# Kernel tuning notes

Hardware: AMD Instinct MI355X
Metric: run time of the kernel (lower is better)

## Reference

```python
import jax, jax.numpy as jnp
import numpy as np
import math

B, L, D, NH, FF, NL = 4, 512, 512, 8, 2048, 4
DS, DC, DI, DTR = 64, 4, 1024, 32  # mamba: d_state, d_conv, d_inner=2*D, dt_rank=ceil(D/16)
HD = D // NH


def _layer_norm(x, g, b):
    m = x.mean(-1, keepdims=True)
    v = ((x - m) ** 2).mean(-1, keepdims=True)
    return (x - m) / jnp.sqrt(v + 1e-5) * g + b


def _pos_encode(x):
    Lx, Dx = x.shape[1], x.shape[2]
    pos = jnp.arange(Lx, dtype=jnp.float32)[:, None]
    div = jnp.exp(jnp.arange(0, Dx, 2, dtype=jnp.float32) * (-math.log(10000.0) / Dx))
    ang = pos * div  # (L, D/2)
    pe = jnp.stack([jnp.sin(ang), jnp.cos(ang)], -1).reshape(Lx, Dx)  # interleaved sin/cos
    return x + pe[None]


def _mha(x, w_qkv, b_qkv, w_o, b_o):
    Bx, Lx, Dx = x.shape
    qkv = x @ w_qkv.T + b_qkv
    q, k, v = jnp.split(qkv, 3, -1)
    heads = lambda t: t.reshape(Bx, Lx, NH, HD).transpose(0, 2, 1, 3)
    q, k, v = heads(q), heads(k), heads(v)
    s = jnp.einsum('bhqd,bhkd->bhqk', q, k) / math.sqrt(HD)
    p = jax.nn.softmax(s, -1)
    o = jnp.einsum('bhqk,bhkd->bhqd', p, v).transpose(0, 2, 1, 3).reshape(Bx, Lx, Dx)
    return o @ w_o.T + b_o


def _mamba(x, in_w, conv_w, conv_b, xproj_w, dt_w, dt_b, A_log, D_skip, out_w):
    Bx, Lx, _ = x.shape
    xz = x @ in_w.T  # (B, L, 2*DI)
    xc, z = jnp.split(xz, 2, -1)
    # depthwise causal conv1d
    xc = jax.lax.conv_general_dilated(xc.transpose(0, 2, 1), conv_w[:, None, :], (1,), [(DC - 1, 0)], feature_group_count=DI, dimension_numbers=('NCH', 'OIH', 'NCH'))
    xc = jax.nn.silu((xc + conv_b[None, :, None]).transpose(0, 2, 1))  # (B, L, DI)
    x_dbl = xc @ xproj_w.T
    dt, Bm, Cm = jnp.split(x_dbl, [DTR, DTR + DS], -1)
    dt = jax.nn.softplus(dt @ dt_w.T + dt_b)  # (B, L, DI)
    A = -jnp.exp(A_log)  # (DI, DS)

    def step(h, t):
        dt_t, B_t, C_t, u_t = t  # (B,DI),(B,DS),(B,DS),(B,DI)
        h = jnp.exp(dt_t[:, :, None] * A) * h + (dt_t * u_t)[:, :, None] * B_t[:, None, :]
        return h, jnp.einsum('bdn,bn->bd', h, C_t)

    h0 = jnp.zeros((Bx, DI, DS), x.dtype)
    xs = (dt.transpose(1, 0, 2), Bm.transpose(1, 0, 2), Cm.transpose(1, 0, 2), xc.transpose(1, 0, 2))
    _, ys = jax.lax.scan(step, h0, xs)
    y = ys.transpose(1, 0, 2) + xc * D_skip
    y = y * jax.nn.silu(z)
    return y @ out_w.T


def setup_inputs():
    key = jax.random.key(0)
    ks = iter(jax.random.split(key, 32))
    def rn(shape, s=0.02):
        return jax.random.normal(next(ks), shape, jnp.float32) * s
    return dict(
        src=jax.random.normal(next(ks), (B, L, D), jnp.float32),
        attn_w_qkv=rn((NL, 3 * D, D)), attn_b_qkv=jnp.zeros((NL, 3 * D)),
        attn_w_o=rn((NL, D, D)), attn_b_o=jnp.zeros((NL, D)),
        ffn_w1=rn((NL, FF, D)), ffn_b1=jnp.zeros((NL, FF)),
        ffn_w2=rn((NL, D, FF)), ffn_b2=jnp.zeros((NL, D)),
        norm1_g=jnp.ones((NL, D)), norm1_b=jnp.zeros((NL, D)),
        in_proj_w=rn((NL, 2 * DI, D)), conv_w=rn((NL, DI, DC), 0.2), conv_b=jnp.zeros((NL, DI)),
        x_proj_w=rn((NL, DTR + 2 * DS, DI)), dt_proj_w=rn((NL, DI, DTR), 0.1), dt_proj_b=jnp.full((NL, DI), -4.0),
        A_log=jnp.broadcast_to(jnp.log(jnp.arange(1, DS + 1, dtype=jnp.float32)), (NL, DI, DS)) + 0.0,
        D_skip=jnp.ones((NL, DI)), out_proj_w=rn((NL, D, DI)),
        normf_g=jnp.ones((D,)), normf_b=jnp.zeros((D,)))


def reference(src, attn_w_qkv, attn_b_qkv, attn_w_o, attn_b_o, ffn_w1, ffn_b1, ffn_w2, ffn_b2, norm1_g, norm1_b, in_proj_w, conv_w, conv_b, x_proj_w, dt_proj_w, dt_proj_b, A_log, D_skip, out_proj_w, normf_g, normf_b):
    x = _pos_encode(src)
    for i in range(NL):
        a = _mha(x, attn_w_qkv[i], attn_b_qkv[i], attn_w_o[i], attn_b_o[i])
        m = _mamba(x, in_proj_w[i], conv_w[i], conv_b[i], x_proj_w[i], dt_proj_w[i], dt_proj_b[i], A_log[i], D_skip[i], out_proj_w[i])
        h = a + m
        h = jax.nn.relu(h @ ffn_w1[i].T + ffn_b1[i]) @ ffn_w2[i].T + ffn_b2[i]
        x = _layer_norm(h, norm1_g[i], norm1_b[i])  # norm1(dropout(ffn(attn+mamba))), dropout=identity
    return _layer_norm(x, normf_g, normf_b)
```

## Files before the change

### kernel.cpp

```cpp
#include <hip/hip_runtime.h>
#include <cmath>


typedef __attribute__((ext_vector_type(8))) __bf16 bf16x8;
typedef __attribute__((ext_vector_type(4))) __bf16 bf16x4;
typedef __attribute__((ext_vector_type(4))) float f32x4;

#define DEV static __device__ __forceinline__

DEV float wave_sum(float x) {
#pragma unroll
  for (int o = 32; o; o >>= 1) x += __shfl_xor(x, o, 64);
  return x;
}
DEV float wave_max(float x) {
#pragma unroll
  for (int o = 32; o; o >>= 1) x = fmaxf(x, __shfl_xor(x, o, 64));
  return x;
}

__global__ void cvt_kernel(const float* __restrict__ s, __bf16* __restrict__ d, int n4) {
  int i = blockIdx.x * 256 + threadIdx.x;
  if (i < n4) {
    float4 v = ((const float4*)s)[i];
    bf16x4 r = {(__bf16)v.x, (__bf16)v.y, (__bf16)v.z, (__bf16)v.w};
    *(bf16x4*)(d + (size_t)i * 4) = r;
  }
}

__global__ void pe_kernel(const float* __restrict__ src, __bf16* __restrict__ xb) {
  int idx = blockIdx.x * 256 + threadIdx.x;
  int d = idx & 511;
  int l = (idx >> 9) & 511;
  float ang = (float)l * expf((float)(d & ~1) * (-9.210340371976184f / 512.f));
  float pe = (d & 1) ? cosf(ang) : sinf(ang);
  xb[idx] = (__bf16)(src[idx] + pe);
}

struct GemmArgs {
  const __bf16* A; const __bf16* W;
  const float* bias; const float* add;
  float* Cf; __bf16* Cb;
  long long sAzb, sAzh, sWzb, sWzh, sADzb, sADzh, sCfzb, sCfzh, sCbzb, sCbzh;
  int lda, ldw, ldad, ldcf, ldcb;
  int M, N, K, ZH;
  float alpha; int act;
  int ct;
};

__global__ __launch_bounds__(64) void gemm_kernel(GemmArgs g) {
  const int lane = threadIdx.x;
  const int m0 = blockIdx.x * 64, n0 = blockIdx.y * 64;
  const int zb = blockIdx.z / g.ZH, zh = blockIdx.z % g.ZH;
  const __bf16* A = g.A + zb * g.sAzb + zh * g.sAzh;
  const __bf16* W = g.W + zb * g.sWzb + zh * g.sWzh;
  const int fr = lane & 15;
  const int fk = (lane >> 4) * 8;
  const __bf16* pa[4]; const __bf16* pw[4];
#pragma unroll
  for (int i = 0; i < 4; ++i) {
    int ra = m0 + i * 16 + fr;
    pa[i] = A + (size_t)ra * g.lda + fk;
    int rw = n0 + i * 16 + fr; if (rw > g.N - 1) rw = g.N - 1;
    pw[i] = W + (size_t)rw * g.ldw + fk;
  }
  f32x4 acc[4][4] = {};
  for (int k0 = 0; k0 < g.K; k0 += 32) {
    bf16x8 af[4], wf[4];
#pragma unroll
    for (int i = 0; i < 4; ++i) af[i] = *(const bf16x8*)(pa[i] + k0);
#pragma unroll
    for (int j = 0; j < 4; ++j) wf[j] = *(const bf16x8*)(pw[j] + k0);
#pragma unroll
    for (int i = 0; i < 4; ++i)
#pragma unroll
      for (int j = 0; j < 4; ++j)
        acc[i][j] = __builtin_amdgcn_mfma_f32_16x16x32_bf16(af[i], wf[j], acc[i][j], 0, 0, 0);
  }
  const float* addp = g.add ? g.add + zb * g.sADzb + zh * g.sADzh : nullptr;
  float* cf = g.Cf ? g.Cf + zb * g.sCfzb + zh * g.sCfzh : nullptr;
  __bf16* cb = g.Cb ? g.Cb + zb * g.sCbzb + zh * g.sCbzh : nullptr;
  const int rbase = m0 + (lane >> 4) * 4;
#pragma unroll
  for (int i = 0; i < 4; ++i) {
#pragma unroll
    for (int j = 0; j < 4; ++j) {
      int col = n0 + j * 16 + fr;
      if (col < g.N) {
#pragma unroll
        for (int r = 0; r < 4; ++r) {
          int row = rbase + i * 16 + r;
          float v = acc[i][j][r] * g.alpha;
          if (g.bias) v += g.bias[col];
          if (addp) v += addp[(size_t)row * g.ldad + col];
          if (g.act == 1) v = fmaxf(v, 0.f);
          else if (g.act == 2) v = (v > 20.f) ? v : log1pf(expf(v));
          if (cf) {
            if (g.ct) cf[(size_t)col * g.ldcf + row] = v;
            else      cf[(size_t)row * g.ldcf + col] = v;
          }
          if (cb) cb[(size_t)row * g.ldcb + col] = (__bf16)v;
        }
      }
    }
  }
}

static void launch_gemm(hipStream_t st,
    const __bf16* A, int lda, long long sAzb, long long sAzh,
    const __bf16* W, int ldw, long long sWzb, long long sWzh,
    const float* bias,
    const float* add, int ldad, long long sADzb, long long sADzh,
    float* Cf, int ldcf, long long sCfzb, long long sCfzh,
    __bf16* Cb, int ldcb, long long sCbzb, long long sCbzh,
    int M, int N, int K, int Z, int ZH, float alpha, int act, int ct = 0) {
  GemmArgs g;
  g.A = A; g.W = W; g.bias = bias; g.add = add; g.Cf = Cf; g.Cb = Cb;
  g.sAzb = sAzb; g.sAzh = sAzh; g.sWzb = sWzb; g.sWzh = sWzh;
  g.sADzb = sADzb; g.sADzh = sADzh; g.sCfzb = sCfzb; g.sCfzh = sCfzh;
  g.sCbzb = sCbzb; g.sCbzh = sCbzh;
  g.lda = lda; g.ldw = ldw; g.ldad = ldad; g.ldcf = ldcf; g.ldcb = ldcb;
  g.M = M; g.N = N; g.K = K; g.ZH = ZH; g.alpha = alpha; g.act = act; g.ct = ct;
  dim3 grid(M / 64, (N + 63) / 64, Z);
  gemm_kernel<<<grid, 64, 0, st>>>(g);
}

__global__ __launch_bounds__(256) void gemm_sk_kernel(GemmArgs g) {
  __shared__ float red[2][64 * 66];
  const int tid = threadIdx.x;
  const int lane = tid & 63;
  const int wid = tid >> 6;
  const int m0 = blockIdx.x * 64, n0 = blockIdx.y * 64;
  const int zb = blockIdx.z / g.ZH, zh = blockIdx.z % g.ZH;
  const __bf16* A = g.A + zb * g.sAzb + zh * g.sAzh;
  const __bf16* W = g.W + zb * g.sWzb + zh * g.sWzh;
  const int fr = lane & 15;
  const int fk = (lane >> 4) * 8;
  const int kbase = wid * (g.K >> 2);
  const __bf16* pa[4]; const __bf16* pw[4];
#pragma unroll
  for (int i = 0; i < 4; ++i) {
    int ra = m0 + i * 16 + fr;
    pa[i] = A + (size_t)ra * g.lda + kbase + fk;
    int rw = n0 + i * 16 + fr; if (rw > g.N - 1) rw = g.N - 1;
    pw[i] = W + (size_t)rw * g.ldw + kbase + fk;
  }
  f32x4 acc[4][4] = {};
  const int kend = g.K >> 2;
  for (int k0 = 0; k0 < kend; k0 += 32) {
    bf16x8 af[4], wf[4];
#pragma unroll
    for (int i = 0; i < 4; ++i) af[i] = *(const bf16x8*)(pa[i] + k0);
#pragma unroll
    for (int j = 0; j < 4; ++j) wf[j] = *(const bf16x8*)(pw[j] + k0);
#pragma unroll
    for (int i = 0; i < 4; ++i)
#pragma unroll
      for (int j = 0; j < 4; ++j)
        acc[i][j] = __builtin_amdgcn_mfma_f32_16x16x32_bf16(af[i], wf[j], acc[i][j], 0, 0, 0);
  }
  float* buf0 = &red[0][0];
  float* buf1 = &red[1][0];
  auto store_acc = [&](float* buf) {
#pragma unroll
    for (int i = 0; i < 4; ++i)
#pragma unroll
      for (int j = 0; j < 4; ++j) {
        int rl = i * 16 + ((lane >> 4) << 2);
        int cl = j * 16 + fr;
#pragma unroll
        for (int r = 0; r < 4; ++r) buf[(rl + r) * 66 + cl] = acc[i][j][r];
      }
  };
  auto add_acc = [&](const float* buf) {
#pragma unroll
    for (int i = 0; i < 4; ++i)
#pragma unroll
      for (int j = 0; j < 4; ++j) {
        int rl = i * 16 + ((lane >> 4) << 2);
        int cl = j * 16 + fr;
#pragma unroll
        for (int r = 0; r < 4; ++r) acc[i][j][r] += buf[(rl + r) * 66 + cl];
      }
  };
  if (wid == 1) store_acc(buf0);
  if (wid == 3) store_acc(buf1);
  __syncthreads();
  if (wid == 0) add_acc(buf0);
  if (wid == 2) add_acc(buf1);
  __syncthreads();
  if (wid == 2) store_acc(buf0);
  __syncthreads();
  if (wid == 0) { add_acc(buf0); store_acc(buf0); }
  __syncthreads();
  const int rl = tid >> 2;
  const int c0l = (tid & 3) * 16;
  const int row = m0 + rl;
  const float* addp = g.add ? g.add + zb * g.sADzb + zh * g.sADzh : nullptr;
  float* cf = g.Cf ? g.Cf + zb * g.sCfzb + zh * g.sCfzh : nullptr;
  __bf16* cb = g.Cb ? g.Cb + zb * g.sCbzb + zh * g.sCbzh : nullptr;
  float v[16];
#pragma unroll
  for (int k = 0; k < 16; ++k) {
    float x = buf0[rl * 66 + c0l + k] * g.alpha;
    int col = n0 + c0l + k;
    if (col < g.N) {
      if (g.bias) x += g.bias[col];
      if (addp) x += addp[(size_t)row * g.ldad + col];
      if (g.act == 1) x = fmaxf(x, 0.f);
      else if (g.act == 2) x = (x > 20.f) ? x : log1pf(expf(x));
    }
    v[k] = x;
  }
  if (n0 + c0l + 15 < g.N) {
    if (cf) {
      float* p = cf + (size_t)row * g.ldcf + n0 + c0l;
#pragma unroll
      for (int k = 0; k < 4; ++k) *(float4*)(p + k * 4) = *(float4*)(v + k * 4);
    }
    if (cb) {
      __bf16* p = cb + (size_t)row * g.ldcb + n0 + c0l;
#pragma unroll
      for (int h = 0; h < 2; ++h) {
        bf16x8 r;
#pragma unroll
        for (int k = 0; k < 8; ++k) r[k] = (__bf16)v[h * 8 + k];
        *(bf16x8*)(p + h * 8) = r;
      }
    }
  } else {
#pragma unroll
    for (int k = 0; k < 16; ++k) {
      int col = n0 + c0l + k;
      if (col < g.N) {
        if (cf) cf[(size_t)row * g.ldcf + col] = v[k];
        if (cb) cb[(size_t)row * g.ldcb + col] = (__bf16)v[k];
      }
    }
  }
}

static void launch_gemm_sk(hipStream_t st,
    const __bf16* A, int lda, long long sAzb, long long sAzh,
    const __bf16* W, int ldw, long long sWzb, long long sWzh,
    const float* bias,
    const float* add, int ldad, long long sADzb, long long sADzh,
    float* Cf, int ldcf, long long sCfzb, long long sCfzh,
    __bf16* Cb, int ldcb, long long sCbzb, long long sCbzh,
    int M, int N, int K, int Z, int ZH, float alpha, int act) {
  GemmArgs g;
  g.A = A; g.W = W; g.bias = bias; g.add = add; g.Cf = Cf; g.Cb = Cb;
  g.sAzb = sAzb; g.sAzh = sAzh; g.sWzb = sWzb; g.sWzh = sWzh;
  g.sADzb = sADzb; g.sADzh = sADzh; g.sCfzb = sCfzb; g.sCfzh = sCfzh;
  g.sCbzb = sCbzb; g.sCbzh = sCbzh;
  g.lda = lda; g.ldw = ldw; g.ldad = ldad; g.ldcf = ldcf; g.ldcb = ldcb;
  g.M = M; g.N = N; g.K = K; g.ZH = ZH; g.alpha = alpha; g.act = act; g.ct = 0;
  dim3 grid(M / 64, (N + 63) / 64, Z);
  gemm_sk_kernel<<<grid, 256, 0, st>>>(g);
}

__global__ __launch_bounds__(256) void transpose_v_kernel(const __bf16* __restrict__ qkv,
                                                          __bf16* __restrict__ vt) {
  int bh = blockIdx.x, b = bh >> 3, h = bh & 7;
  const __bf16* s = qkv + (size_t)b * 512 * 1536 + 1024 + h * 64;
  __bf16* dst = vt + (size_t)bh * 64 * 512;
  __shared__ __align__(16) __bf16 tile[64 * 72];
  int tid = threadIdx.x;
  for (int l0 = 0; l0 < 512; l0 += 64) {
    __syncthreads();
#pragma unroll
    for (int it = 0; it < 2; ++it) {
      int idx = tid + it * 256;
      int l = idx >> 3, dc = (idx & 7) * 8;
      *(uint4*)&tile[l * 72 + dc] = *(const uint4*)(s + (size_t)(l0 + l) * 1536 + dc);
    }
    __syncthreads();
#pragma unroll
    for (int it = 0; it < 2; ++it) {
      int idx = tid + it * 256;
      int dd = idx >> 3, lc = (idx & 7) * 8;
      __align__(16) __bf16 tmp[8];
#pragma unroll
      for (int j = 0; j < 8; ++j) tmp[j] = tile[(lc + j) * 72 + dd];
      *(uint4*)(dst + (size_t)dd * 512 + l0 + lc) = *(uint4*)tmp;
    }
  }
}

__global__ __launch_bounds__(256) void softmax_kernel(const float* __restrict__ S,
                                                      __bf16* __restrict__ P) {
  int row = blockIdx.x * 4 + (threadIdx.x >> 6);
  int lane = threadIdx.x & 63;
  const float* sp = S + (size_t)row * 512 + lane * 8;
  float v[8];
  *(float4*)(v) = *(const float4*)(sp);
  *(float4*)(v + 4) = *(const float4*)(sp + 4);
  float m = v[0];
#pragma unroll
  for (int k = 1; k < 8; ++k) m = fmaxf(m, v[k]);
  m = wave_max(m);
  float s = 0.f;
#pragma unroll
  for (int k = 0; k < 8; ++k) { v[k] = __expf(v[k] - m); s += v[k]; }
  s = wave_sum(s);
  float inv = 1.f / s;
  bf16x8 r;
#pragma unroll
  for (int k = 0; k < 8; ++k) r[k] = (__bf16)(v[k] * inv);
  *(bf16x8*)(P + (size_t)row * 512 + lane * 8) = r;
}

__global__ __launch_bounds__(256) void conv_silu_t_kernel(
    const float* __restrict__ xz, const float* __restrict__ cw, const float* __restrict__ cb,
    __bf16* __restrict__ xcb, float* __restrict__ uT, float* __restrict__ s1T) {
  int c0 = blockIdx.x * 64, t0 = blockIdx.y * 64, b = blockIdx.z;
  __shared__ float su[64][65];
  __shared__ float sz[64][65];
  int c = threadIdx.x & 63;
  int tr = threadIdx.x >> 6;
  int ch = c0 + c;
  float w0 = cw[ch * 4 + 0], w1 = cw[ch * 4 + 1], w2 = cw[ch * 4 + 2], w3 = cw[ch * 4 + 3];
  float bias = cb[ch];
#pragma unroll 4
  for (int it = 0; it < 16; ++it) {
    int tt = it * 4 + tr;
    int t = t0 + tt;
    const float* col = xz + (size_t)b * 512 * 2048 + ch;
    float acc = bias;
    if (t >= 3) {
      acc = fmaf(w0, col[(size_t)(t - 3) * 2048], acc);
      acc = fmaf(w1, col[(size_t)(t - 2) * 2048], acc);
      acc = fmaf(w2, col[(size_t)(t - 1) * 2048], acc);
    } else {
      if (t - 3 >= 0) acc = fmaf(w0, col[(size_t)(t - 3) * 2048], acc);
      if (t - 2 >= 0) acc = fmaf(w1, col[(size_t)(t - 2) * 2048], acc);
      if (t - 1 >= 0) acc = fmaf(w2, col[(size_t)(t - 1) * 2048], acc);
    }
    acc = fmaf(w3, col[(size_t)t * 2048], acc);
    float u = acc / (1.f + __expf(-acc));
    su[tt][c] = u;
    xcb[(size_t)(b * 512 + t) * 1024 + ch] = (__bf16)u;
    float zv = col[(size_t)t * 2048 + 1024];
    sz[tt][c] = zv / (1.f + __expf(-zv));
  }
  __syncthreads();
  int c2 = threadIdx.x >> 2;
  int tb = (threadIdx.x & 3) * 16;
  size_t g = (size_t)(c0 + c2) * 2048 + (size_t)b * 512 + t0 + tb;
#pragma unroll
  for (int i = 0; i < 16; ++i) {
    uT[g + i] = su[tb + i][c2];
    s1T[g + i] = sz[tb + i][c2];
  }
}

__global__ __launch_bounds__(256) void scan_p1_kernel(
    const float* __restrict__ dtT, const float* __restrict__ uT,
    const float* __restrict__ xdbl, const float* __restrict__ A_log,
    float* __restrict__ Aprod, float* __restrict__ hend) {
  int w = (blockIdx.x * 256 + threadIdx.x) >> 6;
  int lane = threadIdx.x & 63;
  int c = w & 7, di = (w >> 3) & 1023, b = w >> 13;
  float aL2 = -__expf(A_log[di * 64 + lane]) * 1.4426950408889634f;
  int t0 = c * 64;
  size_t sbase = (size_t)di * 2048 + (size_t)b * 512 + t0;
  const float* dtp = dtT + sbase;
  const float* up = uT + sbase;
  const float* bp = xdbl + ((size_t)(b * 512 + t0)) * 160 + 32 + lane;
  float h = 0.f, sdt = 0.f;
#pragma unroll 8
  for (int s = 0; s < 64; ++s) {
    float dtv = dtp[s];
    float duv = dtv * up[s];
    float Bv = bp[(size_t)s * 160];
    float dec = exp2f(dtv * aL2);
    sdt += dtv;
    h = fmaf(dec, h, duv * Bv);
  }
  size_t o = (size_t)w * 64 + lane;
  Aprod[o] = exp2f(sdt * aL2);
  hend[o] = h;
}

__global__ __launch_bounds__(256) void scan_p2_kernel(
    const float* __restrict__ Aprod, const float* __restrict__ hend,
    float* __restrict__ hstart) {
  int w = (blockIdx.x * 256 + threadIdx.x) >> 6;
  int lane = threadIdx.x & 63;
  float h = 0.f;
  size_t base = (size_t)w * 8 * 64 + lane;
#pragma unroll
  for (int c = 0; c < 8; ++c) {
    size_t o = base + (size_t)c * 64;
    hstart[o] = h;
    h = fmaf(Aprod[o], h, hend[o]);
  }
}

__global__ __launch_bounds__(128) void scan_p3_kernel(
    const float* __restrict__ dtT, const float* __restrict__ uT,
    const float* __restrict__ s1T, const float* __restrict__ xdbl,
    const float* __restrict__ A_log, const float* __restrict__ Dskip,
    const float* __restrict__ hstart, __bf16* __restrict__ yT) {
  __shared__ float Q[2][32][65];
  int wl = threadIdx.x >> 6;
  int w = (blockIdx.x * 128 + threadIdx.x) >> 6;
  int lane = threadIdx.x & 63;
  int c = w & 7, di = (w >> 3) & 1023, b = w >> 13;
  float aL2 = -__expf(A_log[di * 64 + lane]) * 1.4426950408889634f;
  int t0 = c * 64;
  size_t sbase = (size_t)di * 2048 + (size_t)b * 512 + t0;
  const float* dtp = dtT + sbase;
  const float* up = uT + sbase;
  const float* bp = xdbl + ((size_t)(b * 512 + t0)) * 160 + 32 + lane;
  const float* cp = bp + 64;
  float h = hstart[(size_t)w * 64 + lane];
  float y = 0.f;
#pragma unroll 8
  for (int s = 0; s < 32; ++s) {
    float dtv = dtp[s];
    float duv = dtv * up[s];
    float Bv = bp[(size_t)s * 160];
    float Cv = cp[(size_t)s * 160];
    float dec = exp2f(dtv * aL2);
    h = fmaf(dec, h, duv * Bv);
    Q[wl][s][lane] = h * Cv;
  }
  if (lane < 32) {
    const float* row = &Q[wl][lane][0];
    float a0 = 0.f, a1 = 0.f, a2 = 0.f, a3 = 0.f;
#pragma unroll
    for (int k = 0; k < 64; k += 4) {
      a0 += row[k]; a1 += row[k + 1]; a2 += row[k + 2]; a3 += row[k + 3];
    }
    y = (a0 + a1) + (a2 + a3);
  }
#pragma unroll 8
  for (int s = 32; s < 64; ++s) {
    float dtv = dtp[s];
    float duv = dtv * up[s];
    float Bv = bp[(size_t)s * 160];
    float Cv = cp[(size_t)s * 160];
    float dec = exp2f(dtv * aL2);
    h = fmaf(dec, h, duv * Bv);
    Q[wl][s - 32][lane] = h * Cv;
  }
  if (lane >= 32) {
    const float* row = &Q[wl][lane - 32][0];
    float a0 = 0.f, a1 = 0.f, a2 = 0.f, a3 = 0.f;
#pragma unroll
    for (int k = 0; k < 64; k += 4) {
      a0 += row[k]; a1 += row[k + 1]; a2 += row[k + 2]; a3 += row[k + 3];
    }
    y = (a0 + a1) + (a2 + a3);
  }
  float ue = up[lane];
  float s1e = s1T[sbase + lane];
  yT[sbase + lane] = (__bf16)((y + ue * Dskip[di]) * s1e);
}

__global__ __launch_bounds__(256) void transpose_y_kernel(const __bf16* __restrict__ src,
                                                          __bf16* __restrict__ dst) {
  int r0 = blockIdx.x * 64;
  int c0 = blockIdx.y * 64;
  __shared__ __align__(16) __bf16 tile[64 * 72];
  int tid = threadIdx.x;
#pragma unroll
  for (int it = 0; it < 2; ++it) {
    int idx = tid + it * 256;
    int r = idx >> 3, cc = (idx & 7) * 8;
    *(uint4*)&tile[r * 72 + cc] = *(const uint4*)(src + (size_t)(r0 + r) * 2048 + c0 + cc);
  }
  __syncthreads();
#pragma unroll
  for (int it = 0; it < 2; ++it) {
    int idx = tid + it * 256;
    int cr = idx >> 3, rc = (idx & 7) * 8;
    __align__(16) __bf16 tmp[8];
#pragma unroll
    for (int j = 0; j < 8; ++j) tmp[j] = tile[(rc + j) * 72 + cr];
    *(uint4*)(dst + (size_t)(c0 + cr) * 1024 + r0 + rc) = *(uint4*)tmp;
  }
}

__global__ __launch_bounds__(256) void layernorm_kernel(const float* __restrict__ in,
    const float* __restrict__ g, const float* __restrict__ b,
    float* __restrict__ outf, __bf16* __restrict__ outb) {
  int row = blockIdx.x * 4 + (threadIdx.x >> 6);
  int lane = threadIdx.x & 63;
  const float* p = in + (size_t)row * 512 + lane * 8;
  float v[8];
  *(float4*)(v) = *(const float4*)(p);
  *(float4*)(v + 4) = *(const float4*)(p + 4);
  float s = 0.f;
#pragma unroll
  for (int k = 0; k < 8; ++k) s += v[k];
  float mean = wave_sum(s) * (1.f / 512.f);
  float q = 0.f;
#pragma unroll
  for (int k = 0; k < 8; ++k) { float d = v[k] - mean; q += d * d; }
  float var = wave_sum(q) * (1.f / 512.f);
  float rs = rsqrtf(var + 1e-5f);
  float gv[8], bv[8];
  *(float4*)(gv) = *(const float4*)(g + lane * 8);
  *(float4*)(gv + 4) = *(const float4*)(g + lane * 8 + 4);
  *(float4*)(bv) = *(const float4*)(b + lane * 8);
  *(float4*)(bv + 4) = *(const float4*)(b + lane * 8 + 4);
  float o[8];
#pragma unroll
  for (int k = 0; k < 8; ++k) o[k] = (v[k] - mean) * rs * gv[k] + bv[k];
  if (outf) {
    float* op = outf + (size_t)row * 512 + lane * 8;
    *(float4*)(op) = *(const float4*)(o);
    *(float4*)(op + 4) = *(const float4*)(o + 4);
  }
  if (outb) {
    bf16x8 r;
#pragma unroll
    for (int k = 0; k < 8; ++k) r[k] = (__bf16)o[k];
    *(bf16x8*)(outb + (size_t)row * 512 + lane * 8) = r;
  }
}

extern "C" void kernel_launch(void* const* d_in, const int* in_sizes, int n_in,
                              void* d_out, int out_size, void* d_ws, size_t ws_size,
                              hipStream_t stream) {
  const float* src    = (const float*)d_in[0];
  const float* w_qkv  = (const float*)d_in[1];
  const float* b_qkv  = (const float*)d_in[2];
  const float* w_o    = (const float*)d_in[3];
  const float* b_o    = (const float*)d_in[4];
  const float* w1     = (const float*)d_in[5];
  const float* b1     = (const float*)d_in[6];
  const float* w2     = (const float*)d_in[7];
  const float* b2     = (const float*)d_in[8];
  const float* n1g    = (const float*)d_in[9];
  const float* n1b    = (const float*)d_in[10];
  const float* w_in   = (const float*)d_in[11];
  const float* conv_w = (const float*)d_in[12];
  const float* conv_b = (const float*)d_in[13];
  const float* w_xp   = (const float*)d_in[14];
  const float* w_dt   = (const float*)d_in[15];
  const float* b_dt   = (const float*)d_in[16];
  const float* A_log  = (const float*)d_in[17];
  const float* D_skip = (const float*)d_in[18];
  const float* w_out  = (const float*)d_in[19];
  const float* nfg    = (const float*)d_in[20];
  const float* nfb    = (const float*)d_in[21];
  (void)in_sizes; (void)n_in; (void)out_size; (void)ws_size;

  char* ws = (char*)d_ws;
  __bf16* Wqkv = (__bf16*)(ws + 0);
  __bf16* Wo   = (__bf16*)(ws + 6291456);
  __bf16* W1   = (__bf16*)(ws + 8388608);
  __bf16* W2   = (__bf16*)(ws + 16777216);
  __bf16* Win  = (__bf16*)(ws + 25165824);
  __bf16* Wxp  = (__bf16*)(ws + 33554432);
  __bf16* Wdt  = (__bf16*)(ws + 34865152);
  __bf16* Wout = (__bf16*)(ws + 35127296);
  __bf16* xb16 = (__bf16*)(ws + 39321600);
  float*  xf32 = (float*)(ws + 41418752);
  __bf16* qkvb = (__bf16*)(ws + 45613056);
  __bf16* vt   = (__bf16*)(ws + 51904512);
  __bf16* o_b  = (__bf16*)(ws + 54001664);
  float*  a_f  = (float*)(ws + 56098816);
  __bf16* hb   = (__bf16*)(ws + 60293120);
  float*  h2   = (float*)(ws + 62390272);
  float*  Sf    = (float*)(ws + 66584576);
  float*  xzf   = (float*)(ws + 66584576);
  float*  dtT   = (float*)(ws + 66584576);
  float*  hend0 = (float*)(ws + 74973184);
  float*  uT    = (float*)(ws + 83361792);
  float*  s1T   = (float*)(ws + 91750400);
  float*  hstart = (float*)(ws + 45613056);
  __bf16* yT     = (__bf16*)(ws + 60293120);
  __bf16* Pb    = (__bf16*)(ws + 100139008);
  __bf16* xcb   = (__bf16*)(ws + 100139008);
  float*  xdblf = (float*)(ws + 100139008 + 4194304);
  __bf16* xdblb = (__bf16*)(ws + 100139008 + 5505024);
  __bf16* yb    = (__bf16*)(ws + 100139008 + 6160384);
  __bf16* fb    = (__bf16*)(ws + 100139008 + 10354688);
  float*  Aprod = (float*)(ws + 110493696);

  auto cvt = [&](const float* s, __bf16* dptr, long long n) {
    int n4 = (int)(n / 4);
    cvt_kernel<<<(n4 + 255) / 256, 256, 0, stream>>>(s, dptr, n4);
  };
  cvt(w_qkv, Wqkv, 4LL * 1536 * 512);
  cvt(w_o,   Wo,   4LL * 512 * 512);
  cvt(w1,    W1,   4LL * 2048 * 512);
  cvt(w2,    W2,   4LL * 512 * 2048);
  cvt(w_in,  Win,  4LL * 2048 * 512);
  cvt(w_xp,  Wxp,  4LL * 160 * 1024);
  cvt(w_dt,  Wdt,  4LL * 1024 * 32);
  cvt(w_out, Wout, 4LL * 512 * 1024);

  pe_kernel<<<4096, 256, 0, stream>>>(src, xb16);

  for (int i = 0; i < 4; ++i) {
    launch_gemm_sk(stream, xb16, 512, 0, 0, Wqkv + (size_t)i * 1536 * 512, 512, 0, 0,
                   b_qkv + i * 1536, nullptr, 0, 0, 0,
                   nullptr, 0, 0, 0, qkvb, 1536, 0, 0,
                   2048, 1536, 512, 1, 1, 1.f, 0);
    transpose_v_kernel<<<32, 256, 0, stream>>>(qkvb, vt);
    launch_gemm(stream, qkvb, 1536, 512LL * 1536, 64, qkvb + 512, 1536, 512LL * 1536, 64,
                nullptr, nullptr, 0, 0, 0,
                Sf, 512, 2097152LL, 262144LL, nullptr, 0, 0, 0,
                512, 512, 64, 32, 8, 0.125f, 0);
    softmax_kernel<<<4096, 256, 0, stream>>>(Sf, Pb);
    launch_gemm_sk(stream, Pb, 512, 2097152LL, 262144LL, vt, 512, 262144LL, 32768LL,
                   nullptr, nullptr, 0, 0, 0,
                   nullptr, 0, 0, 0, o_b, 512, 262144LL, 64LL,
                   512, 64, 512, 32, 8, 1.f, 0);
    launch_gemm_sk(stream, o_b, 512, 0, 0, Wo + (size_t)i * 512 * 512, 512, 0, 0,
                   b_o + i * 512, nullptr, 0, 0, 0,
                   a_f, 512, 0, 0, nullptr, 0, 0, 0,
                   2048, 512, 512, 1, 1, 1.f, 0);
    launch_gemm_sk(stream, xb16, 512, 0, 0, Win + (size_t)i * 2048 * 512, 512, 0, 0,
                   nullptr, nullptr, 0, 0, 0,
                   xzf, 2048, 0, 0, nullptr, 0, 0, 0,
                   2048, 2048, 512, 1, 1, 1.f, 0);
    conv_silu_t_kernel<<<dim3(16, 8, 4), 256, 0, stream>>>(
        xzf, conv_w + i * 1024 * 4, conv_b + i * 1024, xcb, uT, s1T);
    launch_gemm_sk(stream, xcb, 1024, 0, 0, Wxp + (size_t)i * 160 * 1024, 1024, 0, 0,
                   nullptr, nullptr, 0, 0, 0,
                   xdblf, 160, 0, 0, xdblb, 160, 0, 0,
                   2048, 160, 1024, 1, 1, 1.f, 0);
    launch_gemm(stream, xdblb, 160, 0, 0, Wdt + (size_t)i * 1024 * 32, 32, 0, 0,
                b_dt + i * 1024, nullptr, 0, 0, 0,
                dtT, 2048, 0, 0, nullptr, 0, 0, 0,
                2048, 1024, 32, 1, 1, 1.f, 2, 1);
    scan_p1_kernel<<<8192, 256, 0, stream>>>(dtT, uT, xdblf,
                                             A_log + (size_t)i * 1024 * 64, Aprod, hend0);
    scan_p2_kernel<<<1024, 256, 0, stream>>>(Aprod, hend0, hstart);
    scan_p3_kernel<<<16384, 128, 0, stream>>>(dtT, uT, s1T, xdblf,
                                              A_log + (size_t)i * 1024 * 64,
                                              D_skip + i * 1024, hstart, yT);
    transpose_y_kernel<<<dim3(16, 32), 256, 0, stream>>>(yT, yb);
    launch_gemm_sk(stream, yb, 1024, 0, 0, Wout + (size_t)i * 512 * 1024, 1024, 0, 0,
                   nullptr, a_f, 512, 0, 0,
                   nullptr, 0, 0, 0, hb, 512, 0, 0,
                   2048, 512, 1024, 1, 1, 1.f, 0);
    launch_gemm_sk(stream, hb, 512, 0, 0, W1 + (size_t)i * 2048 * 512, 512, 0, 0,
                   b1 + i * 2048, nullptr, 0, 0, 0,
                   nullptr, 0, 0, 0, fb, 2048, 0, 0,
                   2048, 2048, 512, 1, 1, 1.f, 1);
    launch_gemm_sk(stream, fb, 2048, 0, 0, W2 + (size_t)i * 512 * 2048, 2048, 0, 0,
                   b2 + i * 512, nullptr, 0, 0, 0,
                   h2, 512, 0, 0, nullptr, 0, 0, 0,
                   2048, 512, 2048, 1, 1, 1.f, 0);
    layernorm_kernel<<<512, 256, 0, stream>>>(h2, n1g + i * 512, n1b + i * 512, xf32, xb16);
  }
  layernorm_kernel<<<512, 256, 0, stream>>>(xf32, nfg, nfb, (float*)d_out, nullptr);
}
```

Measured before the change: 1.719 ms.

## Add 8-wave split-K GEMM with LDS tree reduction for narrow-N GEMMs

Adds a 512-thread GEMM variant where each of 8 waves computes a 64x64 tile over one eighth of K. The partial sums are combined through a shared-memory tree reduction before the fused bias, add and activation epilogue. It is applied to the narrow-N GEMMs (PV, output projection, x_proj, Mamba out_proj, FFN2), whose small grids underfill the GPU. In exchange it uses about 67KB of LDS per block and adds several barriers, which may limit occupancy.

```diff
diff --git a/kernel.cpp b/kernel.cpp
--- a/kernel.cpp
+++ b/kernel.cpp
@@ -257,6 +257,139 @@
   g.M = M; g.N = N; g.K = K; g.ZH = ZH; g.alpha = alpha; g.act = act; g.ct = 0;
   dim3 grid(M / 64, (N + 63) / 64, Z);
   gemm_sk_kernel<<<grid, 256, 0, st>>>(g);
+}
+
+__global__ __launch_bounds__(512, 4) void gemm_sk8_kernel(GemmArgs g) {
+  __shared__ float red[4][64 * 66];
+  const int tid = threadIdx.x;
+  const int lane = tid & 63;
+  const int wid = tid >> 6;
+  const int m0 = blockIdx.x * 64, n0 = blockIdx.y * 64;
+  const int zb = blockIdx.z / g.ZH, zh = blockIdx.z % g.ZH;
+  const __bf16* A = g.A + zb * g.sAzb + zh * g.sAzh;
+  const __bf16* W = g.W + zb * g.sWzb + zh * g.sWzh;
+  const int fr = lane & 15;
+  const int fk = (lane >> 4) * 8;
+  const int kbase = wid * (g.K >> 3);
+  const __bf16* pa[4]; const __bf16* pw[4];
+#pragma unroll
+  for (int i = 0; i < 4; ++i) {
+    int ra = m0 + i * 16 + fr;
+    pa[i] = A + (size_t)ra * g.lda + kbase + fk;
+    int rw = n0 + i * 16 + fr; if (rw > g.N - 1) rw = g.N - 1;
+    pw[i] = W + (size_t)rw * g.ldw + kbase + fk;
+  }
+  f32x4 acc[4][4] = {};
+  const int kend = g.K >> 3;
+  for (int k0 = 0; k0 < kend; k0 += 32) {
+    bf16x8 af[4], wf[4];
+#pragma unroll
+    for (int i = 0; i < 4; ++i) af[i] = *(const bf16x8*)(pa[i] + k0);
+#pragma unroll
+    for (int j = 0; j < 4; ++j) wf[j] = *(const bf16x8*)(pw[j] + k0);
+#pragma unroll
+    for (int i = 0; i < 4; ++i)
+#pragma unroll
+      for (int j = 0; j < 4; ++j)
+        acc[i][j] = __builtin_amdgcn_mfma_f32_16x16x32_bf16(af[i], wf[j], acc[i][j], 0, 0, 0);
+  }
+  auto store_acc = [&](float* buf) {
+#pragma unroll
+    for (int i = 0; i < 4; ++i)
+#pragma unroll
+      for (int j = 0; j < 4; ++j) {
+        int rl = i * 16 + ((lane >> 4) << 2);
+        int cl = j * 16 + fr;
+#pragma unroll
+        for (int r = 0; r < 4; ++r) buf[(rl + r) * 66 + cl] = acc[i][j][r];
+      }
+  };
+  auto add_acc = [&](const float* buf) {
+#pragma unroll
+    for (int i = 0; i < 4; ++i)
+#pragma unroll
+      for (int j = 0; j < 4; ++j) {
+        int rl = i * 16 + ((lane >> 4) << 2);
+        int cl = j * 16 + fr;
+#pragma unroll
+        for (int r = 0; r < 4; ++r) acc[i][j][r] += buf[(rl + r) * 66 + cl];
+      }
+  };
+  if (wid & 1) store_acc(&red[wid >> 1][0]);
+  __syncthreads();
+  if (!(wid & 1)) add_acc(&red[wid >> 1][0]);
+  __syncthreads();
+  if (wid == 2) store_acc(&red[0][0]);
+  if (wid == 6) store_acc(&red[1][0]);
+  __syncthreads();
+  if (wid == 0) add_acc(&red[0][0]);
+  if (wid == 4) add_acc(&red[1][0]);
+  __syncthreads();
+  if (wid == 4) store_acc(&red[0][0]);
+  __syncthreads();
+  if (wid == 0) { add_acc(&red[0][0]); store_acc(&red[0][0]); }
+  __syncthreads();
+  const float* buf0 = &red[0][0];
+  const int rl = tid >> 3;
+  const int c0l = (tid & 7) * 8;
+  const int row = m0 + rl;
+  const float* addp = g.add ? g.add + zb * g.sADzb + zh * g.sADzh : nullptr;
+  float* cf = g.Cf ? g.Cf + zb * g.sCfzb + zh * g.sCfzh : nullptr;
+  __bf16* cb = g.Cb ? g.Cb + zb * g.sCbzb + zh * g.sCbzh : nullptr;
+  float v[8];
+#pragma unroll
+  for (int k = 0; k < 8; ++k) {
+    float x = buf0[rl * 66 + c0l + k] * g.alpha;
+    int col = n0 + c0l + k;
+    if (col < g.N) {
+      if (g.bias) x += g.bias[col];
+      if (addp) x += addp[(size_t)row * g.ldad + col];
+      if (g.act == 1) x = fmaxf(x, 0.f);
+      else if (g.act == 2) x = (x > 20.f) ? x : log1pf(expf(x));
+    }
+    v[k] = x;
+  }
+  if (n0 + c0l + 7 < g.N) {
+    if (cf) {
+      float* p = cf + (size_t)row * g.ldcf + n0 + c0l;
+      *(float4*)(p) = *(float4*)(v);
+      *(float4*)(p + 4) = *(float4*)(v + 4);
+    }
+    if (cb) {
+      bf16x8 r;
+#pragma unroll
+      for (int k = 0; k < 8; ++k) r[k] = (__bf16)v[k];
+      *(bf16x8*)(cb + (size_t)row * g.ldcb + n0 + c0l) = r;
+    }
+  } else {
+#pragma unroll
+    for (int k = 0; k < 8; ++k) {
+      int col = n0 + c0l + k;
+      if (col < g.N) {
+        if (cf) cf[(size_t)row * g.ldcf + col] = v[k];
+        if (cb) cb[(size_t)row * g.ldcb + col] = (__bf16)v[k];
+      }
+    }
+  }
+}
+
+static void launch_gemm_sk8(hipStream_t st,
+    const __bf16* A, int lda, long long sAzb, long long sAzh,
+    const __bf16* W, int ldw, long long sWzb, long long sWzh,
+    const float* bias,
+    const float* add, int ldad, long long sADzb, long long sADzh,
+    float* Cf, int ldcf, long long sCfzb, long long sCfzh,
+    __bf16* Cb, int ldcb, long long sCbzb, long long sCbzh,
+    int M, int N, int K, int Z, int ZH, float alpha, int act) {
+  GemmArgs g;
+  g.A = A; g.W = W; g.bias = bias; g.add = add; g.Cf = Cf; g.Cb = Cb;
+  g.sAzb = sAzb; g.sAzh = sAzh; g.sWzb = sWzb; g.sWzh = sWzh;
+  g.sADzb = sADzb; g.sADzh = sADzh; g.sCfzb = sCfzb; g.sCfzh = sCfzh;
+  g.sCbzb = sCbzb; g.sCbzh = sCbzh;
+  g.lda = lda; g.ldw = ldw; g.ldad = ldad; g.ldcf = ldcf; g.ldcb = ldcb;
+  g.M = M; g.N = N; g.K = K; g.ZH = ZH; g.alpha = alpha; g.act = act; g.ct = 0;
+  dim3 grid(M / 64, (N + 63) / 64, Z);
+  gemm_sk8_kernel<<<grid, 512, 0, st>>>(g);
 }
 
 __global__ __launch_bounds__(256) void transpose_v_kernel(const __bf16* __restrict__ qkv,
@@ -608,24 +741,24 @@
                 Sf, 512, 2097152LL, 262144LL, nullptr, 0, 0, 0,
                 512, 512, 64, 32, 8, 0.125f, 0);
     softmax_kernel<<<4096, 256, 0, stream>>>(Sf, Pb);
-    launch_gemm_sk(stream, Pb, 512, 2097152LL, 262144LL, vt, 512, 262144LL, 32768LL,
-                   nullptr, nullptr, 0, 0, 0,
-                   nullptr, 0, 0, 0, o_b, 512, 262144LL, 64LL,
-                   512, 64, 512, 32, 8, 1.f, 0);
-    launch_gemm_sk(stream, o_b, 512, 0, 0, Wo + (size_t)i * 512 * 512, 512, 0, 0,
-                   b_o + i * 512, nullptr, 0, 0, 0,
-                   a_f, 512, 0, 0, nullptr, 0, 0, 0,
-                   2048, 512, 512, 1, 1, 1.f, 0);
+    launch_gemm_sk8(stream, Pb, 512, 2097152LL, 262144LL, vt, 512, 262144LL, 32768LL,
+                    nullptr, nullptr, 0, 0, 0,
+                    nullptr, 0, 0, 0, o_b, 512, 262144LL, 64LL,
+                    512, 64, 512, 32, 8, 1.f, 0);
+    launch_gemm_sk8(stream, o_b, 512, 0, 0, Wo + (size_t)i * 512 * 512, 512, 0, 0,
+                    b_o + i * 512, nullptr, 0, 0, 0,
+                    a_f, 512, 0, 0, nullptr, 0, 0, 0,
+                    2048, 512, 512, 1, 1, 1.f, 0);
     launch_gemm_sk(stream, xb16, 512, 0, 0, Win + (size_t)i * 2048 * 512, 512, 0, 0,
                    nullptr, nullptr, 0, 0, 0,
                    xzf, 2048, 0, 0, nullptr, 0, 0, 0,
                    2048, 2048, 512, 1, 1, 1.f, 0);
     conv_silu_t_kernel<<<dim3(16, 8, 4), 256, 0, stream>>>(
         xzf, conv_w + i * 1024 * 4, conv_b + i * 1024, xcb, uT, s1T);
-    launch_gemm_sk(stream, xcb, 1024, 0, 0, Wxp + (size_t)i * 160 * 1024, 1024, 0, 0,
-                   nullptr, nullptr, 0, 0, 0,
-                   xdblf, 160, 0, 0, xdblb, 160, 0, 0,
-                   2048, 160, 1024, 1, 1, 1.f, 0);
+    launch_gemm_sk8(stream, xcb, 1024, 0, 0, Wxp + (size_t)i * 160 * 1024, 1024, 0, 0,
+                    nullptr, nullptr, 0, 0, 0,
+                    xdblf, 160, 0, 0, xdblb, 160, 0, 0,
+                    2048, 160, 1024, 1, 1, 1.f, 0);
     launch_gemm(stream, xdblb, 160, 0, 0, Wdt + (size_t)i * 1024 * 32, 32, 0, 0,
                 b_dt + i * 1024, nullptr, 0, 0, 0,
                 dtT, 2048, 0, 0, nullptr, 0, 0, 0,
@@ -637,18 +770,18 @@
                                               A_log + (size_t)i * 1024 * 64,
                                               D_skip + i * 1024, hstart, yT);
     transpose_y_kernel<<<dim3(16, 32), 256, 0, stream>>>(yT, yb);
-    launch_gemm_sk(stream, yb, 1024, 0, 0, Wout + (size_t)i * 512 * 1024, 1024, 0, 0,
-                   nullptr, a_f, 512, 0, 0,
-                   nullptr, 0, 0, 0, hb, 512, 0, 0,
-                   2048, 512, 1024, 1, 1, 1.f, 0);
+    launch_gemm_sk8(stream, yb, 1024, 0, 0, Wout + (size_t)i * 512 * 1024, 1024, 0, 0,
+                    nullptr, a_f, 512, 0, 0,
+                    nullptr, 0, 0, 0, hb, 512, 0, 0,
+                    2048, 512, 1024, 1, 1, 1.f, 0);
     launch_gemm_sk(stream, hb, 512, 0, 0, W1 + (size_t)i * 2048 * 512, 512, 0, 0,
                    b1 + i * 2048, nullptr, 0, 0, 0,
                    nullptr, 0, 0, 0, fb, 2048, 0, 0,
                    2048, 2048, 512, 1, 1, 1.f, 1);
-    launch_gemm_sk(stream, fb, 2048, 0, 0, W2 + (size_t)i * 512 * 2048, 2048, 0, 0,
-                   b2 + i * 512, nullptr, 0, 0, 0,
-                   h2, 512, 0, 0, nullptr, 0, 0, 0,
-                   2048, 512, 2048, 1, 1, 1.f, 0);
+    launch_gemm_sk8(stream, fb, 2048, 0, 0, W2 + (size_t)i * 512 * 2048, 2048, 0, 0,
+                    b2 + i * 512, nullptr, 0, 0, 0,
+                    h2, 512, 0, 0, nullptr, 0, 0, 0,
+                    2048, 512, 2048, 1, 1, 1.f, 0);
     layernorm_kernel<<<512, 256, 0, stream>>>(h2, n1g + i * 512, n1b + i * 512, xf32, xb16);
   }
   layernorm_kernel<<<512, 256, 0, stream>>>(xf32, nfg, nfb, (float*)d_out, nullptr);
```

Result: no change. 1.748 ms (+1.7%).

## Fuse QK^T scores with softmax in registers and vectorize scan loads

Applied to the files above, without the earlier changes.

Replaces the separate QK^T GEMM, which wrote fp32 scores to memory, and the softmax kernel with a single kernel. Each wave computes a 16x512 score strip with MFMA directly from the QKV buffer and does the softmax in registers before writing bf16 probabilities. This removes the fp32 score round trip and one launch, at the cost of 128 accumulator registers per lane, uncoalesced scattered bf16 stores, and K fragments loaded from global without LDS reuse. The Mamba scan kernels also load dt and u as float4 with a smaller unroll.

```diff
diff --git a/kernel.cpp b/kernel.cpp
--- a/kernel.cpp
+++ b/kernel.cpp
@@ -259,6 +259,52 @@
   gemm_sk_kernel<<<grid, 256, 0, st>>>(g);
 }
 
+__global__ __launch_bounds__(256) void attn_sm_kernel(const __bf16* __restrict__ qkv,
+                                                      __bf16* __restrict__ P) {
+  const int bh = blockIdx.y, b = bh >> 3, h = bh & 7;
+  const int w = threadIdx.x >> 6, lane = threadIdx.x & 63;
+  const int fr = lane & 15, fk = (lane >> 4) * 8;
+  const __bf16* qb = qkv + (size_t)b * 512 * 1536 + h * 64;
+  const __bf16* kb = qb + 512;
+  const int arow = blockIdx.x * 64 + w * 16 + fr;
+  const __bf16* qp = qb + (size_t)arow * 1536 + fk;
+  f32x4 acc[32];
+#pragma unroll
+  for (int j = 0; j < 32; ++j) acc[j] = (f32x4){0.f, 0.f, 0.f, 0.f};
+#pragma unroll
+  for (int kk = 0; kk < 2; ++kk) {
+    bf16x8 af = *(const bf16x8*)(qp + kk * 32);
+#pragma unroll
+    for (int j = 0; j < 32; ++j) {
+      bf16x8 wf = *(const bf16x8*)(kb + (size_t)(j * 16 + fr) * 1536 + kk * 32 + fk);
+      acc[j] = __builtin_amdgcn_mfma_f32_16x16x32_bf16(af, wf, acc[j], 0, 0, 0);
+    }
+  }
+  __bf16* Pb = P + (size_t)bh * 512 * 512;
+  const int rbase = blockIdx.x * 64 + w * 16 + ((lane >> 4) << 2);
+#pragma unroll
+  for (int r = 0; r < 4; ++r) {
+    float m = -1e30f;
+#pragma unroll
+    for (int j = 0; j < 32; ++j) m = fmaxf(m, acc[j][r]);
+#pragma unroll
+    for (int o = 1; o < 16; o <<= 1) m = fmaxf(m, __shfl_xor(m, o, 64));
+    float s = 0.f;
+#pragma unroll
+    for (int j = 0; j < 32; ++j) {
+      float e = __expf((acc[j][r] - m) * 0.125f);
+      acc[j][r] = e;
+      s += e;
+    }
+#pragma unroll
+    for (int o = 1; o < 16; o <<= 1) s += __shfl_xor(s, o, 64);
+    float inv = 1.f / s;
+    __bf16* prow = Pb + (size_t)(rbase + r) * 512 + fr;
+#pragma unroll
+    for (int j = 0; j < 32; ++j) prow[j * 16] = (__bf16)(acc[j][r] * inv);
+  }
+}
+
 __global__ __launch_bounds__(256) void transpose_v_kernel(const __bf16* __restrict__ qkv,
                                                           __bf16* __restrict__ vt) {
   int bh = blockIdx.x, b = bh >> 3, h = bh & 7;
@@ -285,29 +331,6 @@
       *(uint4*)(dst + (size_t)dd * 512 + l0 + lc) = *(uint4*)tmp;
     }
   }
-}
-
-__global__ __launch_bounds__(256) void softmax_kernel(const float* __restrict__ S,
-                                                      __bf16* __restrict__ P) {
-  int row = blockIdx.x * 4 + (threadIdx.x >> 6);
-  int lane = threadIdx.x & 63;
-  const float* sp = S + (size_t)row * 512 + lane * 8;
-  float v[8];
-  *(float4*)(v) = *(const float4*)(sp);
-  *(float4*)(v + 4) = *(const float4*)(sp + 4);
-  float m = v[0];
-#pragma unroll
-  for (int k = 1; k < 8; ++k) m = fmaxf(m, v[k]);
-  m = wave_max(m);
-  float s = 0.f;
-#pragma unroll
-  for (int k = 0; k < 8; ++k) { v[k] = __expf(v[k] - m); s += v[k]; }
-  s = wave_sum(s);
-  float inv = 1.f / s;
-  bf16x8 r;
-#pragma unroll
-  for (int k = 0; k < 8; ++k) r[k] = (__bf16)(v[k] * inv);
-  *(bf16x8*)(P + (size_t)row * 512 + lane * 8) = r;
 }
 
 __global__ __launch_bounds__(256) void conv_silu_t_kernel(
@@ -368,14 +391,19 @@
   const float* up = uT + sbase;
   const float* bp = xdbl + ((size_t)(b * 512 + t0)) * 160 + 32 + lane;
   float h = 0.f, sdt = 0.f;
-#pragma unroll 8
-  for (int s = 0; s < 64; ++s) {
-    float dtv = dtp[s];
-    float duv = dtv * up[s];
-    float Bv = bp[(size_t)s * 160];
-    float dec = exp2f(dtv * aL2);
-    sdt += dtv;
-    h = fmaf(dec, h, duv * Bv);
+#pragma unroll 2
+  for (int s4 = 0; s4 < 64; s4 += 4) {
+    float4 dt4 = *(const float4*)(dtp + s4);
+    float4 u4 = *(const float4*)(up + s4);
+#pragma unroll
+    for (int q = 0; q < 4; ++q) {
+      float dtv = ((const float*)&dt4)[q];
+      float uv = ((const float*)&u4)[q];
+      float Bv = bp[(size_t)(s4 + q) * 160];
+      float dec = exp2f(dtv * aL2);
+      sdt += dtv;
+      h = fmaf(dec, h, (dtv * uv) * Bv);
+    }
   }
   size_t o = (size_t)w * 64 + lane;
   Aprod[o] = exp2f(sdt * aL2);
@@ -416,15 +444,21 @@
   const float* cp = bp + 64;
   float h = hstart[(size_t)w * 64 + lane];
   float y = 0.f;
-#pragma unroll 8
-  for (int s = 0; s < 32; ++s) {
-    float dtv = dtp[s];
-    float duv = dtv * up[s];
-    float Bv = bp[(size_t)s * 160];
-    float Cv = cp[(size_t)s * 160];
-    float dec = exp2f(dtv * aL2);
-    h = fmaf(dec, h, duv * Bv);
-    Q[wl][s][lane] = h * Cv;
+#pragma unroll 2
+  for (int s4 = 0; s4 < 32; s4 += 4) {
+    float4 dt4 = *(const float4*)(dtp + s4);
+    float4 u4 = *(const float4*)(up + s4);
+#pragma unroll
+    for (int q = 0; q < 4; ++q) {
+      int s = s4 + q;
+      float dtv = ((const float*)&dt4)[q];
+      float uv = ((const float*)&u4)[q];
+      float Bv = bp[(size_t)s * 160];
+      float Cv = cp[(size_t)s * 160];
+      float dec = exp2f(dtv * aL2);
+      h = fmaf(dec, h, (dtv * uv) * Bv);
+      Q[wl][s][lane] = h * Cv;
+    }
   }
   if (lane < 32) {
     const float* row = &Q[wl][lane][0];
@@ -435,15 +469,21 @@
     }
     y = (a0 + a1) + (a2 + a3);
   }
-#pragma unroll 8
-  for (int s = 32; s < 64; ++s) {
-    float dtv = dtp[s];
-    float duv = dtv * up[s];
-    float Bv = bp[(size_t)s * 160];
-    float Cv = cp[(size_t)s * 160];
-    float dec = exp2f(dtv * aL2);
-    h = fmaf(dec, h, duv * Bv);
-    Q[wl][s - 32][lane] = h * Cv;
+#pragma unroll 2
+  for (int s4 = 32; s4 < 64; s4 += 4) {
+    float4 dt4 = *(const float4*)(dtp + s4);
+    float4 u4 = *(const float4*)(up + s4);
+#pragma unroll
+    for (int q = 0; q < 4; ++q) {
+      int s = s4 + q;
+      float dtv = ((const float*)&dt4)[q];
+      float uv = ((const float*)&u4)[q];
+      float Bv = bp[(size_t)s * 160];
+      float Cv = cp[(size_t)s * 160];
+      float dec = exp2f(dtv * aL2);
+      h = fmaf(dec, h, (dtv * uv) * Bv);
+      Q[wl][s - 32][lane] = h * Cv;
+    }
   }
   if (lane >= 32) {
     const float* row = &Q[wl][lane - 32][0];
@@ -566,7 +606,6 @@
   float*  a_f  = (float*)(ws + 56098816);
   __bf16* hb   = (__bf16*)(ws + 60293120);
   float*  h2   = (float*)(ws + 62390272);
-  float*  Sf    = (float*)(ws + 66584576);
   float*  xzf   = (float*)(ws + 66584576);
   float*  dtT   = (float*)(ws + 66584576);
   float*  hend0 = (float*)(ws + 74973184);
@@ -603,11 +642,7 @@
                    nullptr, 0, 0, 0, qkvb, 1536, 0, 0,
                    2048, 1536, 512, 1, 1, 1.f, 0);
     transpose_v_kernel<<<32, 256, 0, stream>>>(qkvb, vt);
-    launch_gemm(stream, qkvb, 1536, 512LL * 1536, 64, qkvb + 512, 1536, 512LL * 1536, 64,
-                nullptr, nullptr, 0, 0, 0,
-                Sf, 512, 2097152LL, 262144LL, nullptr, 0, 0, 0,
-                512, 512, 64, 32, 8, 0.125f, 0);
-    softmax_kernel<<<4096, 256, 0, stream>>>(Sf, Pb);
+    attn_sm_kernel<<<dim3(8, 32), 256, 0, stream>>>(qkvb, Pb);
     launch_gemm_sk(stream, Pb, 512, 2097152LL, 262144LL, vt, 512, 262144LL, 32768LL,
                    nullptr, nullptr, 0, 0, 0,
                    nullptr, 0, 0, 0, o_b, 512, 262144LL, 64LL,
```

Result: faster. 1.655 ms (-3.7%).
